# Optimization experiments

Hardware: AMD Instinct MI355X
Metric: run time of the kernel (lower is better)

Reference implementation:

```python
import jax, jax.numpy as jnp
import numpy as np

NPERSEG = 128
HOP = 64  # nperseg - noverlap, noverlap = nperseg//2
NFRAMES = 33
NFREQ = 65

def _hann_periodic(n):
    # scipy get_window('hann', n) -> periodic (sym=False) hann window
    return 0.5 - 0.5 * jnp.cos(2.0 * jnp.pi * jnp.arange(n, dtype=jnp.float32) / n)

def setup_inputs() -> dict:
    key = jax.random.key(0)
    ks = jax.random.split(key, 10)
    B, L, S = 2048, 2048, 8
    H = 1024
    return {
        "x": jax.random.normal(ks[0], (B, L, S), dtype=jnp.float32),
        "sensor_weights": jnp.ones((S,), dtype=jnp.float32),
        "W1": jax.random.normal(ks[1], (H, 2145), dtype=jnp.float32) * 0.02,
        "b1": jnp.zeros((H,), dtype=jnp.float32),
        "W2": jax.random.normal(ks[2], (H // 2, H), dtype=jnp.float32) * 0.02,
        "b2": jnp.zeros((H // 2,), dtype=jnp.float32),
        "W3": jax.random.normal(ks[3], (H // 4, H // 2), dtype=jnp.float32) * 0.02,
        "b3": jnp.zeros((H // 4,), dtype=jnp.float32),
        "W4": jax.random.normal(ks[4], (10, H // 4), dtype=jnp.float32) * 0.02,
        "b4": jnp.zeros((10,), dtype=jnp.float32),
    }

def _stft_mag(x):
    # x: (B, L, S) -> |STFT| per sensor: (B, S, NFREQ, NFRAMES), matching scipy.signal.stft defaults
    xs = jnp.transpose(x, (0, 2, 1))  # (B, S, L)
    # boundary='zeros': pad nperseg//2 zeros each side -> L + 128 = 2176, exact multiple (padded=True adds nothing)
    xp = jnp.pad(xs, ((0, 0), (0, 0), (NPERSEG // 2, NPERSEG // 2)))
    idx = jnp.arange(NFRAMES)[:, None] * HOP + jnp.arange(NPERSEG)[None, :]  # (33, 128)
    frames = xp[:, :, idx]  # (B, S, 33, 128)
    win = _hann_periodic(NPERSEG)
    spec = jnp.fft.rfft(frames * win, axis=-1)  # (B, S, 33, 65)
    mag = jnp.abs(spec) / jnp.sum(win)
    return jnp.transpose(mag, (0, 1, 3, 2))  # (B, S, 65, 33) = (B, S, freq, time)

def reference(x, sensor_weights, W1, b1, W2, b2, W3, b3, W4, b4):
    B = x.shape[0]
    mag = _stft_mag(x)  # (B, S, F, T)
    w = jax.nn.softmax(sensor_weights)  # (S,)
    fused = jnp.einsum('s,bsft->bft', w, mag)  # weighted sensor fusion
    h = fused.reshape(B, -1)  # (B, 2145)
    h = jax.nn.relu(h @ W1.T + b1)
    h = jax.nn.relu(h @ W2.T + b2)
    h = jax.nn.relu(h @ W3.T + b3)
    return h @ W4.T + b4
```

## Files before the change

kernel.cpp:

```cpp
#include <hip/hip_runtime.h>
#include <hip/hip_bf16.h>
#include <math.h>

#define NPERSEG 128
#define HOP     64
#define NFRAMES 33
#define NFREQ   65
#define BATCH   2048
#define LEN     2048
#define NSENS   8
#define FEAT    (NFREQ * NFRAMES)
#define FEATP   2176
#define H1      1024
#define H2      512
#define H3      256
#define NOUT    10

#define XROW    2264
#define MT_PER_WAVE 3
#define NCWS    (10 * 4 * 64 * 8)

typedef __attribute__((ext_vector_type(8))) short short8;
typedef __attribute__((ext_vector_type(4))) float float4v;
typedef unsigned short ushort;
typedef unsigned int uint;

__device__ __forceinline__ ushort f2b(float v) {
    __hip_bfloat16 h = __float2bfloat16(v);
    return *reinterpret_cast<ushort*>(&h);
}
__device__ __forceinline__ uint pack2(float a, float b) {
    return (uint)f2b(a) | ((uint)f2b(b) << 16);
}
__device__ __forceinline__ float b2fu(uint lo16) {
    union { uint i; float f; } c; c.i = lo16 << 16; return c.f;
}
__device__ __forceinline__ void gl_lds16(const void* g, void* l) {
    __builtin_amdgcn_global_load_lds(
        (const __attribute__((address_space(1))) unsigned int*)g,
        (__attribute__((address_space(3))) unsigned int*)l, 16, 0, 0);
}

__global__ __launch_bounds__(256)
void sf_prep(const float* __restrict__ W1, const float* __restrict__ W2,
             const float* __restrict__ W3,
             ushort* __restrict__ cws, ushort* __restrict__ W1b,
             ushort* __restrict__ W2b, ushort* __restrict__ W3b) {
    const int N1 = NCWS;
    const int N2 = N1 + H1 * FEATP;
    const int N3 = N2 + H2 * H1;
    const int N4 = N3 + H3 * H2;
    int e = blockIdx.x * 256 + threadIdx.x;
    const float STEP = 6.28318530717958647692f / 128.0f;
    if (e < N1) {
        int j = e & 7, l = (e >> 3) & 63, ks = (e >> 9) & 3, tile = e >> 11;
        int n = tile * 16 + (l & 15);
        int k = ks * 32 + (l >> 4) * 8 + j;
        float win = 0.5f - 0.5f * cosf(STEP * (float)k);
        float v = 0.f;
        if (n < NFREQ)
            v = win * cosf(STEP * (float)((n * k) & 127)) * (1.0f / 64.0f);
        else if (n >= 80 && n < 80 + NFREQ)
            v = win * sinf(STEP * (float)(((n - 80) * k) & 127)) * (1.0f / 64.0f);
        cws[e] = f2b(v);
    } else if (e < N2) {
        int e2 = e - N1;
        int n = e2 / FEATP, k = e2 - n * FEATP;
        W1b[e2] = f2b(k < FEAT ? W1[(long)n * FEAT + k] : 0.f);
    } else if (e < N3) {
        int e2 = e - N2;
        W2b[e2] = f2b(W2[e2]);
    } else if (e < N4) {
        int e2 = e - N3;
        W3b[e2] = f2b(W3[e2]);
    }
}

__global__ __launch_bounds__(512, 4)
void sf_stft_fuse(const float* __restrict__ x,
                  const float* __restrict__ sw,
                  const ushort* __restrict__ cws,
                  ushort* __restrict__ h0) {
    __shared__ __align__(16) ushort xbp[NSENS * XROW];
    __shared__ __align__(16) ushort hstage[FEATP];

    const int b    = blockIdx.x;
    const int tid  = threadIdx.x;
    const int lane = tid & 63;
    const int wv   = tid >> 6;

    const float4* xb4 = (const float4*)(x + (size_t)b * (LEN * NSENS));
    uint* xw = (uint*)xbp;
    for (int e = tid; e < 2048; e += 512) {
        int i = e >> 1;
        int h = e & 1;
        float4 v0 = xb4[i * 4 + h];
        float4 v1 = xb4[i * 4 + 2 + h];
        int base = (h * 4) * (XROW / 2) + 32 + i;
        xw[base                 ] = pack2(v0.x, v1.x);
        xw[base +     (XROW / 2)] = pack2(v0.y, v1.y);
        xw[base + 2 * (XROW / 2)] = pack2(v0.z, v1.z);
        xw[base + 3 * (XROW / 2)] = pack2(v0.w, v1.w);
    }
    for (int e = tid; e < NSENS * 32; e += 512)
        xw[(e >> 5) * (XROW / 2) + (e & 31)] = 0;
    for (int e = tid; e < NSENS * 76; e += 512) {
        int s = e / 76;
        xw[s * (XROW / 2) + 1056 + (e - s * 76)] = 0;
    }
    if (tid < FEATP - FEAT) hstage[FEAT + tid] = 0;
    __syncthreads();

    const int col = lane & 15;
    const int q   = lane >> 4;

    float wqa[4];
    {
        float s0 = sw[0], s1 = sw[1], s2 = sw[2], s3 = sw[3];
        float s4 = sw[4], s5 = sw[5], s6 = sw[6], s7 = sw[7];
        float mx = fmaxf(fmaxf(fmaxf(s0, s1), fmaxf(s2, s3)),
                         fmaxf(fmaxf(s4, s5), fmaxf(s6, s7)));
        float e0 = expf(s0 - mx), e1 = expf(s1 - mx), e2 = expf(s2 - mx), e3 = expf(s3 - mx);
        float e4 = expf(s4 - mx), e5 = expf(s5 - mx), e6 = expf(s6 - mx), e7 = expf(s7 - mx);
        float inv = 1.0f / (e0 + e1 + e2 + e3 + e4 + e5 + e6 + e7);
        if ((q & 1) == 0) { wqa[0] = e0 * inv; wqa[1] = e1 * inv; wqa[2] = e2 * inv; wqa[3] = e3 * inv; }
        else              { wqa[0] = e4 * inv; wqa[1] = e5 * inv; wqa[2] = e6 * inv; wqa[3] = e7 * inv; }
    }

    const ushort* abase[MT_PER_WAVE];
    #pragma unroll
    for (int mb = 0; mb < MT_PER_WAVE; ++mb) {
        int mi = wv * MT_PER_WAVE + mb;
        int m  = mi * 16 + col;
        int ta = m >> 3; if (ta > NFRAMES) ta = NFRAMES;
        int sa = m & 7;
        abase[mb] = &xbp[sa * XROW + ta * HOP + q * 8];
    }

    ushort* h0b = h0 + (size_t)b * FEATP;
    #pragma unroll 1
    for (int np = 0; np < 5; ++np) {
        float4v accR[MT_PER_WAVE], accI[MT_PER_WAVE];
        #pragma unroll
        for (int mb = 0; mb < MT_PER_WAVE; ++mb) {
            accR[mb] = (float4v){0.f, 0.f, 0.f, 0.f};
            accI[mb] = (float4v){0.f, 0.f, 0.f, 0.f};
        }
        #pragma unroll
        for (int ks = 0; ks < 4; ++ks) {
            short8 bR = *(const short8*)&cws[(((np * 4) + ks) * 64 + lane) * 8];
            short8 bI = *(const short8*)&cws[((((np + 5) * 4) + ks) * 64 + lane) * 8];
            #pragma unroll
            for (int mb = 0; mb < MT_PER_WAVE; ++mb) {
                short8 af = *(const short8*)(abase[mb] + ks * 32);
                accR[mb] = __builtin_amdgcn_mfma_f32_16x16x32_bf16(af, bR, accR[mb], 0, 0, 0);
                accI[mb] = __builtin_amdgcn_mfma_f32_16x16x32_bf16(af, bI, accI[mb], 0, 0, 0);
            }
        }
        int f = np * 16 + col;
        #pragma unroll
        for (int mb = 0; mb < MT_PER_WAVE; ++mb) {
            float ps = 0.f;
            #pragma unroll
            for (int r = 0; r < 4; ++r) {
                float re = accR[mb][r];
                float im = accI[mb][r];
                ps += wqa[r] * sqrtf(re * re + im * im);
            }
            float tot = ps + __shfl_xor(ps, 16, 64);
            int mi = wv * MT_PER_WAVE + mb;
            int t  = mi * 2 + (q >> 1);
            if (((q & 1) == 0) && t < NFRAMES && f < NFREQ)
                hstage[f * NFRAMES + t] = f2b(tot);
        }
    }
    __syncthreads();

    const uint2* hsw = (const uint2*)hstage;
    uint2* ho = (uint2*)(h0b);
    for (int e = tid; e < FEATP / 4; e += 512)
        ho[e] = hsw[e];
}

template <int MT, int RELU>
__global__ __launch_bounds__(64)
void sf_gemm1w(const ushort* __restrict__ A, const ushort* __restrict__ W,
               const float* __restrict__ bias, ushort* __restrict__ C,
               int M, int N, int K) {
    const int BM = MT * 16;
    __shared__ __align__(16) ushort As[2][BM * 64];
    __shared__ __align__(16) ushort Bs[2][64 * 64];

    const int lane = threadIdx.x;
    const int col  = lane & 15;
    const int q    = lane >> 4;
    const int m0 = blockIdx.y * BM;
    const int n0 = blockIdx.x * 64;

    const int srow = lane >> 3;
    const int skch = (lane & 7) ^ srow;

    const ushort* ag = A + (size_t)(m0 + srow) * K + skch * 8;
    const ushort* wg = W + (size_t)(n0 + srow) * K + skch * 8;

    float4v acc[MT][4];
    #pragma unroll
    for (int mi = 0; mi < MT; ++mi)
        #pragma unroll
        for (int ni = 0; ni < 4; ++ni)
            acc[mi][ni] = (float4v){0.f, 0.f, 0.f, 0.f};

    #pragma unroll
    for (int i = 0; i < MT * 2; ++i)
        gl_lds16(ag + (size_t)(8 * i) * K, &As[0][i * 512]);
    #pragma unroll
    for (int i = 0; i < 8; ++i)
        gl_lds16(wg + (size_t)(8 * i) * K, &Bs[0][i * 512]);

    const int nk = K >> 6;
    const int fs = col & 7;
    for (int kt = 0; kt < nk; ++kt) {
        const int buf = kt & 1;
        short8 afr[2][MT], bfr[2][4];
        #pragma unroll
        for (int ks = 0; ks < 2; ++ks) {
            #pragma unroll
            for (int mi = 0; mi < MT; ++mi)
                afr[ks][mi] = *(const short8*)&As[buf][(mi * 16 + col) * 64 + (((ks * 4 + q) ^ fs) * 8)];
            #pragma unroll
            for (int ni = 0; ni < 4; ++ni)
                bfr[ks][ni] = *(const short8*)&Bs[buf][(ni * 16 + col) * 64 + (((ks * 4 + q) ^ fs) * 8)];
        }
        if (kt + 1 < nk) {
            const size_t ko = (size_t)(kt + 1) * 64;
            #pragma unroll
            for (int i = 0; i < MT * 2; ++i)
                gl_lds16(ag + (size_t)(8 * i) * K + ko, &As[buf ^ 1][i * 512]);
            #pragma unroll
            for (int i = 0; i < 8; ++i)
                gl_lds16(wg + (size_t)(8 * i) * K + ko, &Bs[buf ^ 1][i * 512]);
        }
        #pragma unroll
        for (int ks = 0; ks < 2; ++ks)
            #pragma unroll
            for (int mi = 0; mi < MT; ++mi)
                #pragma unroll
                for (int ni = 0; ni < 4; ++ni)
                    acc[mi][ni] = __builtin_amdgcn_mfma_f32_16x16x32_bf16(
                        afr[ks][mi], bfr[ks][ni], acc[mi][ni], 0, 0, 0);
    }

    #pragma unroll
    for (int ni = 0; ni < 4; ++ni) {
        int n = n0 + ni * 16 + col;
        float bn = bias[n];
        #pragma unroll
        for (int mi = 0; mi < MT; ++mi) {
            int mbase = m0 + mi * 16 + q * 4;
            #pragma unroll
            for (int r = 0; r < 4; ++r) {
                float v = acc[mi][ni][r] + bn;
                if (RELU) v = fmaxf(v, 0.f);
                C[(size_t)(mbase + r) * N + n] = f2b(v);
            }
        }
    }
}

__global__ __launch_bounds__(256)
void sf_final(const ushort* __restrict__ h3, const float* __restrict__ W4,
              const float* __restrict__ b4, float* __restrict__ out) {
    int o = blockIdx.x * 256 + threadIdx.x;
    if (o >= BATCH * NOUT) return;
    int m = o / NOUT, n = o - m * NOUT;
    const uint2*  av  = (const uint2*)(h3 + (size_t)m * H3);
    const float4* wv4 = (const float4*)(W4 + (size_t)n * H3);
    float s = 0.f;
    #pragma unroll 8
    for (int j = 0; j < H3 / 4; ++j) {
        uint2 a = av[j];
        float4 w = wv4[j];
        s = fmaf(b2fu(a.x & 0xffffu), w.x, s);
        s = fmaf(b2fu(a.x >> 16),     w.y, s);
        s = fmaf(b2fu(a.y & 0xffffu), w.z, s);
        s = fmaf(b2fu(a.y >> 16),     w.w, s);
    }
    out[o] = s + b4[n];
}

extern "C" void kernel_launch(void* const* d_in, const int* in_sizes, int n_in,
                              void* d_out, int out_size, void* d_ws, size_t ws_size,
                              hipStream_t stream) {
    const float* x  = (const float*)d_in[0];
    const float* sw = (const float*)d_in[1];
    const float* W1 = (const float*)d_in[2];
    const float* b1 = (const float*)d_in[3];
    const float* W2 = (const float*)d_in[4];
    const float* b2 = (const float*)d_in[5];
    const float* W3 = (const float*)d_in[6];
    const float* b3 = (const float*)d_in[7];
    const float* W4 = (const float*)d_in[8];
    const float* b4 = (const float*)d_in[9];
    float* out = (float*)d_out;

    char* cur = (char*)d_ws;
    ushort* cws  = (ushort*)cur;                cur += (size_t)NCWS * 2;
    ushort* h0   = (ushort*)cur;                cur += (size_t)BATCH * FEATP * 2;
    ushort* W1b  = (ushort*)cur;                cur += (size_t)H1 * FEATP * 2;
    ushort* W2b  = (ushort*)cur;                cur += (size_t)H2 * H1 * 2;
    ushort* W3b  = (ushort*)cur;                cur += (size_t)H3 * H2 * 2;
    ushort* h1   = (ushort*)cur;                cur += (size_t)BATCH * H1 * 2;
    ushort* h2   = (ushort*)cur;                cur += (size_t)BATCH * H2 * 2;
    ushort* h3   = (ushort*)cur;                cur += (size_t)BATCH * H3 * 2;

    const int n_prep = NCWS + H1 * FEATP + H2 * H1 + H3 * H2;
    sf_prep<<<(n_prep + 255) / 256, 256, 0, stream>>>(W1, W2, W3, cws, W1b, W2b, W3b);

    sf_stft_fuse<<<BATCH, 512, 0, stream>>>(x, sw, cws, h0);

    sf_gemm1w<4, 1><<<dim3(H1 / 64, BATCH / 64), 64, 0, stream>>>(h0, W1b, b1, h1, BATCH, H1, FEATP);
    sf_gemm1w<4, 1><<<dim3(H2 / 64, BATCH / 64), 64, 0, stream>>>(h1, W2b, b2, h2, BATCH, H2, H1);
    sf_gemm1w<2, 1><<<dim3(H3 / 64, BATCH / 32), 64, 0, stream>>>(h2, W3b, b3, h3, BATCH, H3, H2);
    sf_final<<<(BATCH * NOUT + 255) / 256, 256, 0, stream>>>(h3, W4, b4, out);
}
```

Measured before the change: 297.4 us.

## Pre-swizzle weights into MFMA fragment layout and drop LDS staging in GEMMs

Weights are converted at prep time into a fragment-major bf16 layout, so each lane loads its B operand directly from global memory with one 16-byte read. The GEMM kernels drop LDS double-buffering and read A and B straight from global/L2 with no staging. The GEMM2/GEMM3 tiles become narrower, giving more blocks. The bf16 conversion and sqrt are replaced with cheaper bit-twiddling and intrinsic versions. Without LDS reuse and async prefetch, global load latency may be exposed, and repeated A reads across N-tiles depend on cache hits.

```diff
diff --git a/kernel.cpp b/kernel.cpp
--- a/kernel.cpp
+++ b/kernel.cpp
@@ -26,8 +26,9 @@
 typedef unsigned int uint;
 
 __device__ __forceinline__ ushort f2b(float v) {
-    __hip_bfloat16 h = __float2bfloat16(v);
-    return *reinterpret_cast<ushort*>(&h);
+    union { float f; uint i; } c; c.f = v;
+    uint r = c.i + 0x7fffu + ((c.i >> 16) & 1u);
+    return (ushort)(r >> 16);
 }
 __device__ __forceinline__ uint pack2(float a, float b) {
     return (uint)f2b(a) | ((uint)f2b(b) << 16);
@@ -35,21 +36,29 @@
 __device__ __forceinline__ float b2fu(uint lo16) {
     union { uint i; float f; } c; c.i = lo16 << 16; return c.f;
 }
-__device__ __forceinline__ void gl_lds16(const void* g, void* l) {
-    __builtin_amdgcn_global_load_lds(
-        (const __attribute__((address_space(1))) unsigned int*)g,
-        (__attribute__((address_space(3))) unsigned int*)l, 16, 0, 0);
+
+__device__ __forceinline__ void frag_cvt(const float* __restrict__ src,
+                                         ushort* __restrict__ dst,
+                                         int e, int KC, int Ksrc) {
+    int j    = e & 7;
+    int lane = (e >> 3) & 63;
+    int rest = e >> 9;
+    int kc   = rest % KC;
+    int nt   = rest / KC;
+    int n = nt * 16 + (lane & 15);
+    int k = kc * 32 + ((lane >> 4) & 3) * 8 + j;
+    dst[e] = f2b(k < Ksrc ? src[(long)n * Ksrc + k] : 0.f);
 }
 
 __global__ __launch_bounds__(256)
 void sf_prep(const float* __restrict__ W1, const float* __restrict__ W2,
              const float* __restrict__ W3,
-             ushort* __restrict__ cws, ushort* __restrict__ W1b,
-             ushort* __restrict__ W2b, ushort* __restrict__ W3b) {
+             ushort* __restrict__ cws, ushort* __restrict__ W1f,
+             ushort* __restrict__ W2f, ushort* __restrict__ W3f) {
     const int N1 = NCWS;
-    const int N2 = N1 + H1 * FEATP;
-    const int N3 = N2 + H2 * H1;
-    const int N4 = N3 + H3 * H2;
+    const int N2 = N1 + (H1 / 16) * (FEATP / 32) * 512;
+    const int N3 = N2 + (H2 / 16) * (H1 / 32) * 512;
+    const int N4 = N3 + (H3 / 16) * (H2 / 32) * 512;
     int e = blockIdx.x * 256 + threadIdx.x;
     const float STEP = 6.28318530717958647692f / 128.0f;
     if (e < N1) {
@@ -64,15 +73,11 @@
             v = win * sinf(STEP * (float)(((n - 80) * k) & 127)) * (1.0f / 64.0f);
         cws[e] = f2b(v);
     } else if (e < N2) {
-        int e2 = e - N1;
-        int n = e2 / FEATP, k = e2 - n * FEATP;
-        W1b[e2] = f2b(k < FEAT ? W1[(long)n * FEAT + k] : 0.f);
+        frag_cvt(W1, W1f, e - N1, FEATP / 32, FEAT);
     } else if (e < N3) {
-        int e2 = e - N2;
-        W2b[e2] = f2b(W2[e2]);
+        frag_cvt(W2, W2f, e - N2, H1 / 32, H1);
     } else if (e < N4) {
-        int e2 = e - N3;
-        W3b[e2] = f2b(W3[e2]);
+        frag_cvt(W3, W3f, e - N3, H2 / 32, H2);
     }
 }
 
@@ -137,7 +142,6 @@
         abase[mb] = &xbp[sa * XROW + ta * HOP + q * 8];
     }
 
-    ushort* h0b = h0 + (size_t)b * FEATP;
     #pragma unroll 1
     for (int np = 0; np < 5; ++np) {
         float4v accR[MT_PER_WAVE], accI[MT_PER_WAVE];
@@ -165,7 +169,7 @@
             for (int r = 0; r < 4; ++r) {
                 float re = accR[mb][r];
                 float im = accI[mb][r];
-                ps += wqa[r] * sqrtf(re * re + im * im);
+                ps += wqa[r] * __builtin_amdgcn_sqrtf(re * re + im * im);
             }
             float tot = ps + __shfl_xor(ps, 16, 64);
             int mi = wv * MT_PER_WAVE + mb;
@@ -177,82 +181,54 @@
     __syncthreads();
 
     const uint2* hsw = (const uint2*)hstage;
-    uint2* ho = (uint2*)(h0b);
+    uint2* ho = (uint2*)(h0 + (size_t)b * FEATP);
     for (int e = tid; e < FEATP / 4; e += 512)
         ho[e] = hsw[e];
 }
 
-template <int MT, int RELU>
+template <int MT, int NT, int RELU>
 __global__ __launch_bounds__(64)
-void sf_gemm1w(const ushort* __restrict__ A, const ushort* __restrict__ W,
-               const float* __restrict__ bias, ushort* __restrict__ C,
-               int M, int N, int K) {
-    const int BM = MT * 16;
-    __shared__ __align__(16) ushort As[2][BM * 64];
-    __shared__ __align__(16) ushort Bs[2][64 * 64];
-
+void sf_gemm_flat(const ushort* __restrict__ A, const ushort* __restrict__ Wf,
+                  const float* __restrict__ bias, ushort* __restrict__ C,
+                  int M, int N, int K) {
+    const int KC = K >> 5;
     const int lane = threadIdx.x;
     const int col  = lane & 15;
     const int q    = lane >> 4;
-    const int m0 = blockIdx.y * BM;
-    const int n0 = blockIdx.x * 64;
-
-    const int srow = lane >> 3;
-    const int skch = (lane & 7) ^ srow;
-
-    const ushort* ag = A + (size_t)(m0 + srow) * K + skch * 8;
-    const ushort* wg = W + (size_t)(n0 + srow) * K + skch * 8;
-
-    float4v acc[MT][4];
+
+    const int m0  = blockIdx.y * (MT * 16);
+    const int nt0 = blockIdx.x * NT;
+
+    const ushort* ab = A + (size_t)(m0 + col) * K + q * 8;
+    const ushort* bb = Wf + ((size_t)nt0 * KC) * 512 + lane * 8;
+
+    float4v acc[MT][NT];
     #pragma unroll
     for (int mi = 0; mi < MT; ++mi)
         #pragma unroll
-        for (int ni = 0; ni < 4; ++ni)
+        for (int ni = 0; ni < NT; ++ni)
             acc[mi][ni] = (float4v){0.f, 0.f, 0.f, 0.f};
 
+    #pragma unroll 2
+    for (int kt = 0; kt < KC; ++kt) {
+        short8 af[MT], bf[NT];
+        #pragma unroll
+        for (int mi = 0; mi < MT; ++mi)
+            af[mi] = *(const short8*)(ab + (size_t)mi * 16 * K + kt * 32);
+        #pragma unroll
+        for (int ni = 0; ni < NT; ++ni)
+            bf[ni] = *(const short8*)(bb + ((size_t)ni * KC + kt) * 512);
+        #pragma unroll
+        for (int mi = 0; mi < MT; ++mi)
+            #pragma unroll
+            for (int ni = 0; ni < NT; ++ni)
+                acc[mi][ni] = __builtin_amdgcn_mfma_f32_16x16x32_bf16(
+                    af[mi], bf[ni], acc[mi][ni], 0, 0, 0);
+    }
+
     #pragma unroll
-    for (int i = 0; i < MT * 2; ++i)
-        gl_lds16(ag + (size_t)(8 * i) * K, &As[0][i * 512]);
-    #pragma unroll
-    for (int i = 0; i < 8; ++i)
-        gl_lds16(wg + (size_t)(8 * i) * K, &Bs[0][i * 512]);
-
-    const int nk = K >> 6;
-    const int fs = col & 7;
-    for (int kt = 0; kt < nk; ++kt) {
-        const int buf = kt & 1;
-        short8 afr[2][MT], bfr[2][4];
-        #pragma unroll
-        for (int ks = 0; ks < 2; ++ks) {
-            #pragma unroll
-            for (int mi = 0; mi < MT; ++mi)
-                afr[ks][mi] = *(const short8*)&As[buf][(mi * 16 + col) * 64 + (((ks * 4 + q) ^ fs) * 8)];
-            #pragma unroll
-            for (int ni = 0; ni < 4; ++ni)
-                bfr[ks][ni] = *(const short8*)&Bs[buf][(ni * 16 + col) * 64 + (((ks * 4 + q) ^ fs) * 8)];
-        }
-        if (kt + 1 < nk) {
-            const size_t ko = (size_t)(kt + 1) * 64;
-            #pragma unroll
-            for (int i = 0; i < MT * 2; ++i)
-                gl_lds16(ag + (size_t)(8 * i) * K + ko, &As[buf ^ 1][i * 512]);
-            #pragma unroll
-            for (int i = 0; i < 8; ++i)
-                gl_lds16(wg + (size_t)(8 * i) * K + ko, &Bs[buf ^ 1][i * 512]);
-        }
-        #pragma unroll
-        for (int ks = 0; ks < 2; ++ks)
-            #pragma unroll
-            for (int mi = 0; mi < MT; ++mi)
-                #pragma unroll
-                for (int ni = 0; ni < 4; ++ni)
-                    acc[mi][ni] = __builtin_amdgcn_mfma_f32_16x16x32_bf16(
-                        afr[ks][mi], bfr[ks][ni], acc[mi][ni], 0, 0, 0);
-    }
-
-    #pragma unroll
-    for (int ni = 0; ni < 4; ++ni) {
-        int n = n0 + ni * 16 + col;
+    for (int ni = 0; ni < NT; ++ni) {
+        int n = nt0 * 16 + ni * 16 + col;
         float bn = bias[n];
         #pragma unroll
         for (int mi = 0; mi < MT; ++mi) {
@@ -306,20 +282,20 @@
     char* cur = (char*)d_ws;
     ushort* cws  = (ushort*)cur;                cur += (size_t)NCWS * 2;
     ushort* h0   = (ushort*)cur;                cur += (size_t)BATCH * FEATP * 2;
-    ushort* W1b  = (ushort*)cur;                cur += (size_t)H1 * FEATP * 2;
-    ushort* W2b  = (ushort*)cur;                cur += (size_t)H2 * H1 * 2;
-    ushort* W3b  = (ushort*)cur;                cur += (size_t)H3 * H2 * 2;
+    ushort* W1f  = (ushort*)cur;                cur += (size_t)H1 * FEATP * 2;
+    ushort* W2f  = (ushort*)cur;                cur += (size_t)H2 * H1 * 2;
+    ushort* W3f  = (ushort*)cur;                cur += (size_t)H3 * H2 * 2;
     ushort* h1   = (ushort*)cur;                cur += (size_t)BATCH * H1 * 2;
     ushort* h2   = (ushort*)cur;                cur += (size_t)BATCH * H2 * 2;
     ushort* h3   = (ushort*)cur;                cur += (size_t)BATCH * H3 * 2;
 
     const int n_prep = NCWS + H1 * FEATP + H2 * H1 + H3 * H2;
-    sf_prep<<<(n_prep + 255) / 256, 256, 0, stream>>>(W1, W2, W3, cws, W1b, W2b, W3b);
+    sf_prep<<<(n_prep + 255) / 256, 256, 0, stream>>>(W1, W2, W3, cws, W1f, W2f, W3f);
 
     sf_stft_fuse<<<BATCH, 512, 0, stream>>>(x, sw, cws, h0);
 
-    sf_gemm1w<4, 1><<<dim3(H1 / 64, BATCH / 64), 64, 0, stream>>>(h0, W1b, b1, h1, BATCH, H1, FEATP);
-    sf_gemm1w<4, 1><<<dim3(H2 / 64, BATCH / 64), 64, 0, stream>>>(h1, W2b, b2, h2, BATCH, H2, H1);
-    sf_gemm1w<2, 1><<<dim3(H3 / 64, BATCH / 32), 64, 0, stream>>>(h2, W3b, b3, h3, BATCH, H3, H2);
+    sf_gemm_flat<4, 4, 1><<<dim3(H1 / 64, BATCH / 64), 64, 0, stream>>>(h0, W1f, b1, h1, BATCH, H1, FEATP);
+    sf_gemm_flat<4, 2, 1><<<dim3(H2 / 32, BATCH / 64), 64, 0, stream>>>(h1, W2f, b2, h2, BATCH, H2, H1);
+    sf_gemm_flat<2, 2, 1><<<dim3(H3 / 32, BATCH / 32), 64, 0, stream>>>(h2, W3f, b3, h3, BATCH, H3, H2);
     sf_final<<<(BATCH * NOUT + 255) / 256, 256, 0, stream>>>(h3, W4, b4, out);
 }
```

Result: slower. 313.0 us (+5.2%).
